# Kernel optimization log

Measured on AMD Instinct MI355X. Metric: run time of the kernel, lower is better.

## Reference

```python
import jax, jax.numpy as jnp
import numpy as np

SR = 24000          # sampling_rate
MAX_H = 60          # min(n_harmonics=100, 60)


def _interp_linear(x, T):
    """Linear upsample along axis 1, align_corners=True. x: [B, C, F] -> [B, T, F]."""
    B, C, F = x.shape
    src = jnp.arange(T, dtype=x.dtype) * ((C - 1) / (T - 1))
    i0 = jnp.clip(jnp.floor(src).astype(jnp.int32), 0, C - 2)
    frac = (src - i0.astype(x.dtype))[None, :, None]
    return x[:, i0, :] * (1.0 - frac) + x[:, i0 + 1, :] * frac


def setup_inputs() -> dict:
    key = jax.random.key(0)
    k1, k2, k3, k4, k5 = jax.random.split(key, 5)
    B, T, H, C, NF = 8, 48000, MAX_H, 100, 5
    f0 = 100.0 + 300.0 * jax.random.uniform(k1, (B, T, 1), dtype=jnp.float32)
    amplitudes = jax.random.uniform(k2, (B, T, H), dtype=jnp.float32)
    formant_freqs = 200.0 + 3300.0 * jax.random.uniform(k3, (B, C, NF), dtype=jnp.float32)
    formant_bws = 50.0 + 150.0 * jax.random.uniform(k4, (B, C, NF), dtype=jnp.float32)
    formant_amps = jax.random.uniform(k5, (B, C, NF), dtype=jnp.float32)
    initial_phase = jnp.zeros((B, 1, 1), dtype=jnp.float32)
    return {"f0": f0, "amplitudes": amplitudes, "formant_freqs": formant_freqs,
            "formant_bws": formant_bws, "formant_amps": formant_amps,
            "initial_phase": initial_phase}


def reference(f0, amplitudes, formant_freqs, formant_bws, formant_amps, initial_phase):
    B, T, _ = f0.shape
    f0 = jax.lax.stop_gradient(f0)                    # torch: f0.detach()
    voiced = (f0[..., 0] > 0).astype(f0.dtype)        # [B, T]
    phase = jnp.cumsum(2.0 * np.pi * f0 / SR, axis=1) + initial_phase  # [B, T, 1]

    ff = _interp_linear(formant_freqs, T)             # [B, T, NF]
    fb = _interp_linear(formant_bws, T)
    fa = _interp_linear(formant_amps, T)

    h = jnp.arange(1, MAX_H + 1, dtype=f0.dtype)      # [H]
    h_freq = f0 * h                                   # [B, T, H]
    nyq = (h_freq < SR / 2).astype(f0.dtype)          # [B, T, H]

    # formant resonance factor: prod over formants of (1 + amp*bw^2/((h_freq-freq)^2+bw^2))
    factor = jnp.ones_like(h_freq)
    for f in range(ff.shape[-1]):                     # NF = 5, small fixed loop
        freq = ff[:, :, f:f + 1]
        bw = fb[:, :, f:f + 1]
        amp = fa[:, :, f:f + 1]
        factor = factor * (1.0 + amp * bw * bw / ((h_freq - freq) ** 2 + bw * bw))

    osc = jnp.sin(phase * h)                          # [B, T, H]
    signal = jnp.sum(osc * amplitudes * factor * nyq, axis=-1) * voiced  # [B, T]

    final_phase = jax.lax.stop_gradient(phase[:, -1:, :] % (2.0 * np.pi))  # [B, 1, 1]
    return signal, final_phase
```

## Files before the change

### kernel.cpp

```cpp
#include <hip/hip_runtime.h>
#include <math.h>

#define SRATE   24000.0
#define NB      8
#define NT      48000
#define NH      60
#define NC      100
#define NFMT    5
#define CTS     64
#define NCH     (NT / CTS)
#define TWO_PI  6.283185307179586476925286766559
#define PSC     (1.0f / 1024.0f)
#define NYQS    11.71875f

typedef float v2f __attribute__((ext_vector_type(2)));

__global__ __launch_bounds__(256) void k_partial(const float* __restrict__ f0,
                                                 double* __restrict__ part) {
    int b = blockIdx.y;
    int ch = blockIdx.x * 4 + (threadIdx.x >> 6);
    int lane = threadIdx.x & 63;
    if (ch < NCH) {
        int t = ch * CTS + lane;
        double q = (double)f0[b * NT + t];
        #pragma unroll
        for (int off = 32; off > 0; off >>= 1)
            q += __shfl_down(q, off, 64);
        if (lane == 0) part[b * NCH + ch] = q;
    }
}

__global__ __launch_bounds__(256) void k_main(const float* __restrict__ f0,
                                              const float* __restrict__ amps,
                                              const float* __restrict__ ffq,
                                              const float* __restrict__ fbw,
                                              const float* __restrict__ fam,
                                              const float* __restrict__ initp,
                                              const double* __restrict__ part,
                                              float* __restrict__ out) {
    int b = blockIdx.y;
    int wv = threadIdx.x >> 6;
    int ch = blockIdx.x * 4 + wv;
    int lane = threadIdx.x & 63;
    if (ch >= NCH) return;
    int t0 = ch * CTS;
    int g0 = lane >> 2, j = lane & 3;
    const float4 f4z = make_float4(0.f, 0.f, 0.f, 0.f);
    const float* ab = amps + (size_t)b * NT * NH;

    __shared__ float coef[4][17][64];

    #define AMPLD(S0, S1, S2, S3, p)                                          \
        { const float4* rr =                                                  \
              (const float4*)(ab + (size_t)(t0 + (p) * 16 + g0) * NH);        \
          S0 = rr[j]; S1 = rr[4 + j]; S2 = rr[8 + j];                         \
          S3 = (j < 3) ? rr[12 + j] : f4z; }

    float4 P0, P1, P2, P3, Q0, Q1, Q2, Q3;
    float4 R0, R1, R2, R3, S0, S1, S2, S3;
    AMPLD(P0, P1, P2, P3, 0)
    AMPLD(Q0, Q1, Q2, Q3, 1)
    AMPLD(R0, R1, R2, R3, 2)
    AMPLD(S0, S1, S2, S3, 3)

    const double* pb = part + b * NCH;
    double sl = 0.0, sa = 0.0;
    #pragma unroll
    for (int k = 0; k < 12; ++k) {
        int idx = k * 64 + lane;
        double v = (idx < NCH) ? pb[idx] : 0.0;
        sa += v;
        if (idx < ch) sl += v;
    }
    #pragma unroll
    for (int off = 1; off < 64; off <<= 1) {
        sl += __shfl_xor(sl, off, 64);
        sa += __shfl_xor(sa, off, 64);
    }

    double initrev = (double)initp[b] * (1.0 / TWO_PI);

    if (ch == 0 && lane == 0) {
        double rv = sa * (1.0 / SRATE) + initrev;
        out[NB * NT + b] = (float)((rv - floor(rv)) * TWO_PI);
    }

    double pfrac = sl * (1.0 / SRATE) + initrev;
    float prefF = (float)(pfrac - floor(pfrac));

    float f0v = f0[b * NT + t0 + lane];
    float incf = f0v;
    #pragma unroll
    for (int off = 1; off < 64; off <<= 1) {
        float n = __shfl_up(incf, off, 64);
        if (lane >= off) incf += n;
    }
    coef[wv][0][lane] = f0v * PSC;
    coef[wv][1][lane] =
        __builtin_amdgcn_fractf(prefF + incf * (1.0f / 24000.0f));

    {
        double srcd = (double)(t0 + lane) * (99.0 / 47999.0);
        int i0 = (int)srcd;
        if (i0 > NC - 2) i0 = NC - 2;
        float frac = (float)(srcd - (double)i0);
        float omf = 1.0f - frac;
        const float* Fq = ffq + (b * NC + i0) * NFMT;
        const float* Bw = fbw + (b * NC + i0) * NFMT;
        const float* Am = fam + (b * NC + i0) * NFMT;
        #pragma unroll
        for (int f = 0; f < NFMT; ++f) {
            float fqv = Fq[f] * omf + Fq[NFMT + f] * frac;
            float bwv = Bw[f] * omf + Bw[NFMT + f] * frac;
            float amv = Am[f] * omf + Am[NFMT + f] * frac;
            float bws = bwv * PSC;
            float c2v = bws * bws;
            coef[wv][2 + f][lane]  = fqv * PSC;
            coef[wv][7 + f][lane]  = amv * c2v;
            coef[wv][12 + f][lane] = c2v;
        }
    }

    auto do_pass = [&](int p, float4 q0, float4 q1, float4 q2, float4 q3) {
        int gp = (p << 4) + g0;
        float f0s   = coef[wv][0][gp];
        float rev_g = coef[wv][1][gp];
        float hb = (float)(j << 2);
        auto sd = [&](float k) {
            return __builtin_amdgcn_sinf(
                __builtin_amdgcn_fractf((hb + k) * rev_g));
        };
        v2f s01 = {sd(1.0f),  sd(2.0f)};
        v2f s23 = {sd(3.0f),  sd(4.0f)};
        v2f s45 = {sd(17.0f), sd(18.0f)};
        v2f s67 = {sd(19.0f), sd(20.0f)};
        float c16 = __builtin_amdgcn_cosf(
            __builtin_amdgcn_fractf(16.0f * rev_g));
        v2f cv = {2.0f * c16, 2.0f * c16};
        v2f s89 = cv * s45 - s01;
        v2f sAB = cv * s67 - s23;
        v2f sCD = cv * s89 - s45;
        v2f sEF = cv * sAB - s67;
        v2f acc2 = {0.0f, 0.0f};
        auto pairf = [&](float h1, v2f sn, float a0, float a1) {
            v2f hfl = {h1, h1 + 1.0f};
            v2f hs = f0s * hfl;
            v2f d0 = hs - coef[wv][2][gp];
            v2f e0 = d0 * d0 + coef[wv][12][gp];
            v2f pN = e0 + coef[wv][7][gp];
            v2f pD = e0;
            #pragma unroll
            for (int f = 1; f < NFMT; ++f) {
                v2f d = hs - coef[wv][2 + f][gp];
                v2f e = d * d + coef[wv][12 + f][gp];
                pN *= e + coef[wv][7 + f][gp];
                pD *= e;
            }
            float R = __builtin_amdgcn_rcpf(pD.x * pD.y);
            v2f fac = {pN.x * pD.y * R, pN.y * pD.x * R};
            v2f fm;
            fm.x = (hs.x < NYQS) ? fac.x : 0.0f;
            fm.y = (hs.y < NYQS) ? fac.y : 0.0f;
            v2f aa = {a0, a1};
            acc2 += (sn * aa) * fm;
        };
        pairf(hb + 1.0f,  s01, q0.x, q0.y);
        pairf(hb + 3.0f,  s23, q0.z, q0.w);
        pairf(hb + 17.0f, s45, q1.x, q1.y);
        pairf(hb + 19.0f, s67, q1.z, q1.w);
        pairf(hb + 33.0f, s89, q2.x, q2.y);
        pairf(hb + 35.0f, sAB, q2.z, q2.w);
        pairf(hb + 49.0f, sCD, q3.x, q3.y);
        pairf(hb + 51.0f, sEF, q3.z, q3.w);
        float acc = acc2.x + acc2.y;
        acc += __shfl_xor(acc, 1, 64);
        acc += __shfl_xor(acc, 2, 64);
        if (j == 0) {
            if (!(f0s > 0.0f)) acc = 0.0f;
            out[b * NT + t0 + (p << 4) + g0] = acc;
        }
    };

    do_pass(0, P0, P1, P2, P3);
    do_pass(1, Q0, Q1, Q2, Q3);
    do_pass(2, R0, R1, R2, R3);
    do_pass(3, S0, S1, S2, S3);
    #undef AMPLD
}

extern "C" void kernel_launch(void* const* d_in, const int* in_sizes, int n_in,
                              void* d_out, int out_size, void* d_ws, size_t ws_size,
                              hipStream_t stream) {
    const float* f0    = (const float*)d_in[0];
    const float* amps  = (const float*)d_in[1];
    const float* ffq   = (const float*)d_in[2];
    const float* fbw   = (const float*)d_in[3];
    const float* fam   = (const float*)d_in[4];
    const float* initp = (const float*)d_in[5];
    float* out = (float*)d_out;

    double* part = (double*)d_ws;

    dim3 gchunk((NCH + 3) / 4, NB);
    k_partial<<<gchunk, 256, 0, stream>>>(f0, part);
    k_main<<<gchunk, 256, 0, stream>>>(f0, amps, ffq, fbw, fam, initp, part, out);
}
```

Before: 34.42 us.

## Split phase prefix into separate kernel and give each wave one 16-step pass

```diff
diff --git a/kernel.cpp b/kernel.cpp
--- a/kernel.cpp
+++ b/kernel.cpp
@@ -30,38 +30,15 @@
     }
 }
 
-__global__ __launch_bounds__(256) void k_main(const float* __restrict__ f0,
-                                              const float* __restrict__ amps,
-                                              const float* __restrict__ ffq,
-                                              const float* __restrict__ fbw,
-                                              const float* __restrict__ fam,
-                                              const float* __restrict__ initp,
-                                              const double* __restrict__ part,
-                                              float* __restrict__ out) {
+__global__ __launch_bounds__(256) void k_rev(const float* __restrict__ f0,
+                                             const double* __restrict__ part,
+                                             const float* __restrict__ initp,
+                                             float2* __restrict__ prep,
+                                             float* __restrict__ outf) {
     int b = blockIdx.y;
-    int wv = threadIdx.x >> 6;
-    int ch = blockIdx.x * 4 + wv;
+    int ch = blockIdx.x * 4 + (threadIdx.x >> 6);
     int lane = threadIdx.x & 63;
     if (ch >= NCH) return;
-    int t0 = ch * CTS;
-    int g0 = lane >> 2, j = lane & 3;
-    const float4 f4z = make_float4(0.f, 0.f, 0.f, 0.f);
-    const float* ab = amps + (size_t)b * NT * NH;
-
-    __shared__ float coef[4][17][64];
-
-    #define AMPLD(S0, S1, S2, S3, p)                                          \
-        { const float4* rr =                                                  \
-              (const float4*)(ab + (size_t)(t0 + (p) * 16 + g0) * NH);        \
-          S0 = rr[j]; S1 = rr[4 + j]; S2 = rr[8 + j];                         \
-          S3 = (j < 3) ? rr[12 + j] : f4z; }
-
-    float4 P0, P1, P2, P3, Q0, Q1, Q2, Q3;
-    float4 R0, R1, R2, R3, S0, S1, S2, S3;
-    AMPLD(P0, P1, P2, P3, 0)
-    AMPLD(Q0, Q1, Q2, Q3, 1)
-    AMPLD(R0, R1, R2, R3, 2)
-    AMPLD(S0, S1, S2, S3, 3)
 
     const double* pb = part + b * NCH;
     double sl = 0.0, sa = 0.0;
@@ -77,115 +54,123 @@
         sl += __shfl_xor(sl, off, 64);
         sa += __shfl_xor(sa, off, 64);
     }
-
     double initrev = (double)initp[b] * (1.0 / TWO_PI);
-
     if (ch == 0 && lane == 0) {
         double rv = sa * (1.0 / SRATE) + initrev;
-        out[NB * NT + b] = (float)((rv - floor(rv)) * TWO_PI);
+        outf[b] = (float)((rv - floor(rv)) * TWO_PI);
     }
-
     double pfrac = sl * (1.0 / SRATE) + initrev;
     float prefF = (float)(pfrac - floor(pfrac));
 
-    float f0v = f0[b * NT + t0 + lane];
+    int t = ch * CTS + lane;
+    float f0v = f0[b * NT + t];
     float incf = f0v;
     #pragma unroll
     for (int off = 1; off < 64; off <<= 1) {
         float n = __shfl_up(incf, off, 64);
         if (lane >= off) incf += n;
     }
-    coef[wv][0][lane] = f0v * PSC;
-    coef[wv][1][lane] =
-        __builtin_amdgcn_fractf(prefF + incf * (1.0f / 24000.0f));
+    float rev = __builtin_amdgcn_fractf(prefF + incf * (1.0f / 24000.0f));
+    prep[(size_t)b * NT + t] = make_float2(f0v * PSC, rev);
+}
 
-    {
-        double srcd = (double)(t0 + lane) * (99.0 / 47999.0);
-        int i0 = (int)srcd;
-        if (i0 > NC - 2) i0 = NC - 2;
-        float frac = (float)(srcd - (double)i0);
-        float omf = 1.0f - frac;
-        const float* Fq = ffq + (b * NC + i0) * NFMT;
-        const float* Bw = fbw + (b * NC + i0) * NFMT;
-        const float* Am = fam + (b * NC + i0) * NFMT;
-        #pragma unroll
-        for (int f = 0; f < NFMT; ++f) {
-            float fqv = Fq[f] * omf + Fq[NFMT + f] * frac;
-            float bwv = Bw[f] * omf + Bw[NFMT + f] * frac;
-            float amv = Am[f] * omf + Am[NFMT + f] * frac;
-            float bws = bwv * PSC;
-            float c2v = bws * bws;
-            coef[wv][2 + f][lane]  = fqv * PSC;
-            coef[wv][7 + f][lane]  = amv * c2v;
-            coef[wv][12 + f][lane] = c2v;
-        }
+__global__ __launch_bounds__(256) void k_main(const float2* __restrict__ prep,
+                                              const float* __restrict__ amps,
+                                              const float* __restrict__ ffq,
+                                              const float* __restrict__ fbw,
+                                              const float* __restrict__ fam,
+                                              float* __restrict__ out) {
+    int b = blockIdx.y;
+    int ch = blockIdx.x;
+    int wv = threadIdx.x >> 6;
+    int lane = threadIdx.x & 63;
+    int g0 = lane >> 2, j = lane & 3;
+    int t = ch * CTS + (wv << 4) + g0;
+
+    const float4* rr = (const float4*)(amps + ((size_t)b * NT + t) * NH);
+    float4 q0 = rr[j];
+    float4 q1 = rr[4 + j];
+    float4 q2 = rr[8 + j];
+    float4 q3 = (j < 3) ? rr[12 + j] : make_float4(0.f, 0.f, 0.f, 0.f);
+    float2 pr = prep[(size_t)b * NT + t];
+
+    double srcd = (double)t * (99.0 / 47999.0);
+    int i0 = (int)srcd;
+    if (i0 > NC - 2) i0 = NC - 2;
+    float frac = (float)(srcd - (double)i0);
+    float omf = 1.0f - frac;
+    const float* Fq = ffq + (b * NC + i0) * NFMT;
+    const float* Bw = fbw + (b * NC + i0) * NFMT;
+    const float* Am = fam + (b * NC + i0) * NFMT;
+    float fq[NFMT], c1[NFMT], c2[NFMT];
+    #pragma unroll
+    for (int f = 0; f < NFMT; ++f) {
+        float fqv = Fq[f] * omf + Fq[NFMT + f] * frac;
+        float bwv = Bw[f] * omf + Bw[NFMT + f] * frac;
+        float amv = Am[f] * omf + Am[NFMT + f] * frac;
+        float bws = bwv * PSC;
+        fq[f] = fqv * PSC;
+        c2[f] = bws * bws;
+        c1[f] = amv * c2[f];
     }
 
-    auto do_pass = [&](int p, float4 q0, float4 q1, float4 q2, float4 q3) {
-        int gp = (p << 4) + g0;
-        float f0s   = coef[wv][0][gp];
-        float rev_g = coef[wv][1][gp];
-        float hb = (float)(j << 2);
-        auto sd = [&](float k) {
-            return __builtin_amdgcn_sinf(
-                __builtin_amdgcn_fractf((hb + k) * rev_g));
-        };
-        v2f s01 = {sd(1.0f),  sd(2.0f)};
-        v2f s23 = {sd(3.0f),  sd(4.0f)};
-        v2f s45 = {sd(17.0f), sd(18.0f)};
-        v2f s67 = {sd(19.0f), sd(20.0f)};
-        float c16 = __builtin_amdgcn_cosf(
-            __builtin_amdgcn_fractf(16.0f * rev_g));
-        v2f cv = {2.0f * c16, 2.0f * c16};
-        v2f s89 = cv * s45 - s01;
-        v2f sAB = cv * s67 - s23;
-        v2f sCD = cv * s89 - s45;
-        v2f sEF = cv * sAB - s67;
-        v2f acc2 = {0.0f, 0.0f};
-        auto pairf = [&](float h1, v2f sn, float a0, float a1) {
-            v2f hfl = {h1, h1 + 1.0f};
-            v2f hs = f0s * hfl;
-            v2f d0 = hs - coef[wv][2][gp];
-            v2f e0 = d0 * d0 + coef[wv][12][gp];
-            v2f pN = e0 + coef[wv][7][gp];
-            v2f pD = e0;
-            #pragma unroll
-            for (int f = 1; f < NFMT; ++f) {
-                v2f d = hs - coef[wv][2 + f][gp];
-                v2f e = d * d + coef[wv][12 + f][gp];
-                pN *= e + coef[wv][7 + f][gp];
-                pD *= e;
-            }
-            float R = __builtin_amdgcn_rcpf(pD.x * pD.y);
-            v2f fac = {pN.x * pD.y * R, pN.y * pD.x * R};
-            v2f fm;
-            fm.x = (hs.x < NYQS) ? fac.x : 0.0f;
-            fm.y = (hs.y < NYQS) ? fac.y : 0.0f;
-            v2f aa = {a0, a1};
-            acc2 += (sn * aa) * fm;
-        };
-        pairf(hb + 1.0f,  s01, q0.x, q0.y);
-        pairf(hb + 3.0f,  s23, q0.z, q0.w);
-        pairf(hb + 17.0f, s45, q1.x, q1.y);
-        pairf(hb + 19.0f, s67, q1.z, q1.w);
-        pairf(hb + 33.0f, s89, q2.x, q2.y);
-        pairf(hb + 35.0f, sAB, q2.z, q2.w);
-        pairf(hb + 49.0f, sCD, q3.x, q3.y);
-        pairf(hb + 51.0f, sEF, q3.z, q3.w);
-        float acc = acc2.x + acc2.y;
-        acc += __shfl_xor(acc, 1, 64);
-        acc += __shfl_xor(acc, 2, 64);
-        if (j == 0) {
-            if (!(f0s > 0.0f)) acc = 0.0f;
-            out[b * NT + t0 + (p << 4) + g0] = acc;
+    float f0s   = pr.x;
+    float rev_g = pr.y;
+
+    float hb = (float)(j << 2);
+    auto sd = [&](float k) {
+        return __builtin_amdgcn_sinf(
+            __builtin_amdgcn_fractf((hb + k) * rev_g));
+    };
+    v2f s01 = {sd(1.0f),  sd(2.0f)};
+    v2f s23 = {sd(3.0f),  sd(4.0f)};
+    v2f s45 = {sd(17.0f), sd(18.0f)};
+    v2f s67 = {sd(19.0f), sd(20.0f)};
+    float c16 = __builtin_amdgcn_cosf(
+        __builtin_amdgcn_fractf(16.0f * rev_g));
+    v2f cv = {2.0f * c16, 2.0f * c16};
+    v2f s89 = cv * s45 - s01;
+    v2f sAB = cv * s67 - s23;
+    v2f sCD = cv * s89 - s45;
+    v2f sEF = cv * sAB - s67;
+    v2f acc2 = {0.0f, 0.0f};
+    auto pairf = [&](float h1, v2f sn, float a0, float a1) {
+        v2f hfl = {h1, h1 + 1.0f};
+        v2f hs = f0s * hfl;
+        v2f d0 = hs - fq[0];
+        v2f e0 = d0 * d0 + c2[0];
+        v2f pN = e0 + c1[0];
+        v2f pD = e0;
+        #pragma unroll
+        for (int f = 1; f < NFMT; ++f) {
+            v2f d = hs - fq[f];
+            v2f e = d * d + c2[f];
+            pN *= e + c1[f];
+            pD *= e;
         }
+        float R = __builtin_amdgcn_rcpf(pD.x * pD.y);
+        v2f fac = {pN.x * pD.y * R, pN.y * pD.x * R};
+        v2f fm;
+        fm.x = (hs.x < NYQS) ? fac.x : 0.0f;
+        fm.y = (hs.y < NYQS) ? fac.y : 0.0f;
+        v2f aa = {a0, a1};
+        acc2 += (sn * aa) * fm;
     };
-
-    do_pass(0, P0, P1, P2, P3);
-    do_pass(1, Q0, Q1, Q2, Q3);
-    do_pass(2, R0, R1, R2, R3);
-    do_pass(3, S0, S1, S2, S3);
-    #undef AMPLD
+    pairf(hb + 1.0f,  s01, q0.x, q0.y);
+    pairf(hb + 3.0f,  s23, q0.z, q0.w);
+    pairf(hb + 17.0f, s45, q1.x, q1.y);
+    pairf(hb + 19.0f, s67, q1.z, q1.w);
+    pairf(hb + 33.0f, s89, q2.x, q2.y);
+    pairf(hb + 35.0f, sAB, q2.z, q2.w);
+    pairf(hb + 49.0f, sCD, q3.x, q3.y);
+    pairf(hb + 51.0f, sEF, q3.z, q3.w);
+    float acc = acc2.x + acc2.y;
+    acc += __shfl_xor(acc, 1, 64);
+    acc += __shfl_xor(acc, 2, 64);
+    if (j == 0) {
+        if (!(f0s > 0.0f)) acc = 0.0f;
+        out[b * NT + t] = acc;
+    }
 }
 
 extern "C" void kernel_launch(void* const* d_in, const int* in_sizes, int n_in,
@@ -200,8 +185,11 @@
     float* out = (float*)d_out;
 
     double* part = (double*)d_ws;
+    float2* prep = (float2*)(part + NB * NCH);
 
     dim3 gchunk((NCH + 3) / 4, NB);
     k_partial<<<gchunk, 256, 0, stream>>>(f0, part);
-    k_main<<<gchunk, 256, 0, stream>>>(f0, amps, ffq, fbw, fam, initp, part, out);
+    k_rev<<<gchunk, 256, 0, stream>>>(f0, part, initp, prep, out + NB * NT);
+    dim3 gmain(NCH, NB);
+    k_main<<<gmain, 256, 0, stream>>>(prep, amps, ffq, fbw, fam, out);
 }
```

New measurement: 37.21 us. +8.1%, slower.
